# Kernel tuning notes

Hardware: AMD Instinct MI355X
Metric: run time of the kernel (lower is better)

## Reference

```python
import jax, jax.numpy as jnp
import numpy as np

N = 50000        # n_nodes
E = 640000       # n_edges
D = 128          # d_model (in_dim == out_dim)
H = 8            # num_heads
DH = D // H      # head dim = 16
EPS = 1e-5


def _batchnorm(x, g, b):
    # BatchNorm1d, training-mode batch statistics (biased variance)
    mu = jnp.mean(x, axis=0)
    var = jnp.mean((x - mu) ** 2, axis=0)
    return (x - mu) * jax.lax.rsqrt(var + EPS) * g + b


def setup_inputs() -> dict:
    key = jax.random.key(0)
    ks = jax.random.split(key, 16)
    s = 0.05
    h = jax.random.normal(ks[0], (N, D), jnp.float32)
    src = jax.random.randint(ks[1], (E,), 0, N)
    # guarantee every node has >= 1 incoming edge (avoids z == 0)
    dst = jnp.concatenate([jnp.arange(N), jax.random.randint(ks[2], (E - N,), 0, N)])
    return {
        "h": h,
        "src": src,
        "dst": dst,
        "WQ": jax.random.normal(ks[3], (D, D), jnp.float32) * s,
        "WK": jax.random.normal(ks[4], (D, D), jnp.float32) * s,
        "WV": jax.random.normal(ks[5], (D, D), jnp.float32) * s,
        "WO": jax.random.normal(ks[6], (D, D), jnp.float32) * s,
        "bO": jnp.zeros((D,), jnp.float32),
        "W1": jax.random.normal(ks[7], (2 * D, D), jnp.float32) * s,
        "b1": jnp.zeros((2 * D,), jnp.float32),
        "W2": jax.random.normal(ks[8], (D, 2 * D), jnp.float32) * s,
        "b2": jnp.zeros((D,), jnp.float32),
        "bn1_g": jnp.ones((D,), jnp.float32),
        "bn1_b": jnp.zeros((D,), jnp.float32),
        "bn2_g": jnp.ones((D,), jnp.float32),
        "bn2_b": jnp.zeros((D,), jnp.float32),
    }


def reference(h, src, dst, WQ, WK, WV, WO, bO, W1, b1, W2, b2, bn1_g, bn1_b, bn2_g, bn2_b):
    n = h.shape[0]
    # projections -> [N, H, DH]
    Q = (h @ WQ.T).reshape(n, H, DH)
    K = (h @ WK.T).reshape(n, H, DH)
    V = (h @ WV.T).reshape(n, H, DH)
    # per-edge score: sum(K[src] * Q[dst]) -> [E, H]; clamp/exp (scaled_exp)
    score = jnp.sum(K[src] * Q[dst], axis=-1) / np.sqrt(DH)
    score = jnp.exp(jnp.clip(score, -5.0, 5.0))
    # scatter-sum weighted values and normalizers to destination nodes
    wV = jax.ops.segment_sum(V[src] * score[..., None], dst, num_segments=n)  # [N,H,DH]
    z = jax.ops.segment_sum(score, dst, num_segments=n)                       # [N,H]
    attn = (wV / z[..., None]).reshape(n, D)
    # O projection + residual + BN1
    h1 = _batchnorm(h + (attn @ WO.T + bO), bn1_g, bn1_b)
    # FFN + residual + BN2
    f = jax.nn.relu(h1 @ W1.T + b1) @ W2.T + b2
    return _batchnorm(h1 + f, bn2_g, bn2_b)
```

## Files before the change

### kernel.cpp

```cpp
#include <hip/hip_runtime.h>
#include <math.h>


#define ND128 16384
typedef _Float16 f16;
typedef __attribute__((ext_vector_type(8))) _Float16 h8;
typedef __attribute__((ext_vector_type(4))) _Float16 h4;
typedef __attribute__((ext_vector_type(2))) _Float16 h2;
typedef __attribute__((ext_vector_type(4))) float f4;
typedef __attribute__((ext_vector_type(2))) float ff2;

__device__ __forceinline__ float fast_exp2(float x) {
#if __has_builtin(__builtin_amdgcn_exp2f)
    return __builtin_amdgcn_exp2f(x);
#else
    return exp2f(x);
#endif
}

template <int CTRL>
__device__ __forceinline__ float dppadd(float x) {
    int t = __builtin_amdgcn_update_dpp(0, __float_as_int(x), CTRL, 0xF, 0xF, false);
    return x + __int_as_float(t);
}
__device__ __forceinline__ float wsum8(float p) {
    p = dppadd<0xB1>(p);
    p = dppadd<0x4E>(p);
    p = dppadd<0x141>(p);
    return p;
}

__device__ __forceinline__ ff2 fp8x2_dec(unsigned v) {
#if __has_builtin(__builtin_amdgcn_cvt_pk_f32_fp8)
    return __builtin_amdgcn_cvt_pk_f32_fp8((int)v, false);
#else
    ff2 r;
    unsigned b0 = v & 0xffu, b1 = (v >> 8) & 0xffu;
    {
        unsigned e = (b0 >> 3) & 15u, m = b0 & 7u;
        float x = e ? __uint_as_float(((e + 120u) << 23) | (m << 20)) : (float)m * 0.001953125f;
        r.x = (b0 & 0x80u) ? -x : x;
    }
    {
        unsigned e = (b1 >> 3) & 15u, m = b1 & 7u;
        float x = e ? __uint_as_float(((e + 120u) << 23) | (m << 20)) : (float)m * 0.001953125f;
        r.y = (b1 & 0x80u) ? -x : x;
    }
    return r;
#endif
}

#if !__has_builtin(__builtin_amdgcn_cvt_pk_fp8_f32)
__device__ __forceinline__ unsigned char fp8_1(float f) {
    float a = fabsf(f);
    unsigned sg = (__float_as_uint(f) >> 31) << 7;
    if (a >= 448.f) return (unsigned char)(sg | 0x7E);
    if (a < 0.0009765625f) return (unsigned char)sg;
    int E; float m = frexpf(a, &E);
    if (E - 1 < -6) {
        int q = (int)rintf(a * 512.f);
        if (q > 7) return (unsigned char)(sg | 0x08);
        return (unsigned char)(sg | q);
    }
    int q = (int)rintf(m * 16.f);
    if (q == 16) { q = 8; E += 1; }
    int Ef = E - 1 + 7;
    if (Ef > 15) return (unsigned char)(sg | 0x7E);
    return (unsigned char)(sg | (Ef << 3) | (q - 8));
}
#endif

__device__ __forceinline__ unsigned fp8_pack4(float a0, float a1, float a2, float a3) {
#if __has_builtin(__builtin_amdgcn_cvt_pk_fp8_f32)
    int pk = __builtin_amdgcn_cvt_pk_fp8_f32(a0, a1, 0, false);
    pk = __builtin_amdgcn_cvt_pk_fp8_f32(a2, a3, pk, true);
    return (unsigned)pk;
#else
    return (unsigned)fp8_1(a0) | ((unsigned)fp8_1(a1) << 8) |
           ((unsigned)fp8_1(a2) << 16) | ((unsigned)fp8_1(a3) << 24);
#endif
}

__global__ __launch_bounds__(256) void k_prep_hist(
    const float* __restrict__ h, f16* __restrict__ hb,
    const float* __restrict__ WQ, const float* __restrict__ WK,
    const float* __restrict__ WV, const float* __restrict__ WO,
    const float* __restrict__ W2,
    f16* __restrict__ Wqb, f16* __restrict__ Wkb,
    f16* __restrict__ Wvb, f16* __restrict__ Wob, f16* __restrict__ W2b,
    int* __restrict__ cursor, const int* __restrict__ dst,
    int N, int E, int nhb)
{
    const int tid = threadIdx.x;
    if (blockIdx.x < (unsigned)nhb) {
        int e = blockIdx.x * 256 + tid;
        if (e < E) atomicAdd(&cursor[dst[e]], 1);
        return;
    }
    const int p = blockIdx.x - nhb;
    const int slab = p >> 1, my = p & 1;
#pragma unroll
    for (int it2 = 0; it2 < 4; ++it2) {
        int it = my * 4 + it2;
        int cid = it * 256 + tid;
        int lane = cid & 63;
        int m = (cid >> 6) & 7;
        int kb = cid >> 9;
        int row = slab * 128 + m * 16 + (lane & 15);
        int col = kb * 32 + (lane >> 4) * 8;
        f16 o8[8];
        if (row < N) {
            const float* pp = h + (size_t)row * 128 + col;
            float4 f0 = *(const float4*)pp;
            float4 f1 = *(const float4*)(pp + 4);
            o8[0] = (f16)f0.x; o8[1] = (f16)f0.y; o8[2] = (f16)f0.z; o8[3] = (f16)f0.w;
            o8[4] = (f16)f1.x; o8[5] = (f16)f1.y; o8[6] = (f16)f1.z; o8[7] = (f16)f1.w;
        } else {
#pragma unroll
            for (int j = 0; j < 8; ++j) o8[j] = (f16)0.f;
        }
        *(h8*)(hb + (size_t)slab * ND128 + (size_t)cid * 8) = *(const h8*)o8;
    }
    if (slab < 6 && my == 1) {
        const float* Wsrc; f16* dstw; int K, base;
        if (slab < 4) {
            Wsrc = slab == 0 ? WQ : slab == 1 ? WK : slab == 2 ? WV : WO;
            dstw = slab == 0 ? Wqb : slab == 1 ? Wkb : slab == 2 ? Wvb : Wob;
            K = 128; base = 0;
        } else {
            Wsrc = W2; dstw = W2b; K = 256; base = (slab - 4) * 2048;
        }
#pragma unroll
        for (int it = 0; it < 8; ++it) {
            int cid = base + it * 256 + tid;
            int lane = cid & 63;
            int kb, nt;
            if (K == 128) { kb = (cid >> 6) & 3; nt = cid >> 8; }
            else          { kb = (cid >> 6) & 7; nt = cid >> 9; }
            int row = nt * 16 + (lane & 15);
            int col = kb * 32 + (lane >> 4) * 8;
            const float* pp = Wsrc + (size_t)row * K + col;
            f16 o8[8];
#pragma unroll
            for (int j = 0; j < 8; ++j) o8[j] = (f16)pp[j];
            *(h8*)(dstw + (size_t)cid * 8) = *(const h8*)o8;
        }
    }
}

__global__ __launch_bounds__(256) void k_qkv(
    const f16* __restrict__ hb, const f16* __restrict__ Wqb,
    const f16* __restrict__ Wkb, const f16* __restrict__ Wvb,
    f16* __restrict__ Qb, unsigned char* __restrict__ KV8, int N)
{
    const int slab = blockIdx.x, oidx = blockIdx.y;
    const int w = threadIdx.x >> 6, lane = threadIdx.x & 63;
    const f16* __restrict__ Wb = oidx == 0 ? Wqb : oidx == 1 ? Wkb : Wvb;
    const f16* A = hb + (size_t)slab * ND128;

    h8 bfr[2][4];
#pragma unroll
    for (int nt = 0; nt < 2; ++nt)
#pragma unroll
        for (int kb = 0; kb < 4; ++kb)
            bfr[nt][kb] = *(const h8*)(Wb + (size_t)(((2 * w + nt) * 4 + kb) * 64 + lane) * 8);

    f4 acc[8][2];
    f4 zero = {0.f, 0.f, 0.f, 0.f};
#pragma unroll
    for (int m = 0; m < 8; ++m) { acc[m][0] = zero; acc[m][1] = zero; }

#pragma unroll
    for (int m = 0; m < 8; ++m) {
#pragma unroll
        for (int kb = 0; kb < 4; ++kb) {
            h8 a = *(const h8*)(A + (size_t)((kb * 8 + m) * 64 + lane) * 8);
            acc[m][0] = __builtin_amdgcn_mfma_f32_16x16x32_f16(bfr[0][kb], a, acc[m][0], 0, 0, 0);
            acc[m][1] = __builtin_amdgcn_mfma_f32_16x16x32_f16(bfr[1][kb], a, acc[m][1], 0, 0, 0);
        }
    }

    const int rl = lane & 15, quad = lane >> 4;
    if (oidx == 0) {
#pragma unroll
        for (int m = 0; m < 8; ++m) {
            int gr = slab * 128 + m * 16 + rl;
            if (gr < N) {
#pragma unroll
                for (int nt = 0; nt < 2; ++nt) {
                    h4 o;
                    o[0] = (f16)acc[m][nt][0]; o[1] = (f16)acc[m][nt][1];
                    o[2] = (f16)acc[m][nt][2]; o[3] = (f16)acc[m][nt][3];
                    *(h4*)(Qb + (size_t)gr * 128 + w * 32 + nt * 16 + quad * 4) = o;
                }
            }
        }
    } else {
        const int voff = (oidx == 2) ? 128 : 0;
#pragma unroll
        for (int m = 0; m < 8; ++m) {
            int gr = slab * 128 + m * 16 + rl;
            if (gr < N) {
#pragma unroll
                for (int nt = 0; nt < 2; ++nt) {
                    unsigned pk = fp8_pack4(acc[m][nt][0], acc[m][nt][1],
                                            acc[m][nt][2], acc[m][nt][3]);
                    *(unsigned*)(KV8 + (size_t)gr * 256 + voff + w * 32 + nt * 16 + quad * 4) = pk;
                }
            }
        }
    }
}

__global__ __launch_bounds__(256) void k_scanA(
    const int* __restrict__ cnt, int* __restrict__ bsum, int N)
{
    const int t = threadIdx.x;
    int base = blockIdx.x * 2048 + t * 8;
    int s = 0;
#pragma unroll
    for (int j = 0; j < 8; ++j) {
        int idx = base + j;
        if (idx < N) s += cnt[idx];
    }
#pragma unroll
    for (int off = 32; off; off >>= 1) s += __shfl_down(s, off, 64);
    __shared__ int ws4[4];
    if ((t & 63) == 0) ws4[t >> 6] = s;
    __syncthreads();
    if (t == 0) bsum[blockIdx.x] = ws4[0] + ws4[1] + ws4[2] + ws4[3];
}

__global__ __launch_bounds__(256) void k_scanC(
    const int* __restrict__ cnt, const int* __restrict__ bsum,
    int* __restrict__ rowptr, int* __restrict__ cursor, int N, int nsb)
{
    const int t = threadIdx.x, b = blockIdx.x;
    __shared__ int sboff;
    if (t == 0) {
        int r = 0;
        for (int i2 = 0; i2 < b; ++i2) r += bsum[i2];
        sboff = r;
    }
    if (t == 64 && b == nsb - 1) {
        int r = 0;
        for (int i2 = 0; i2 < nsb; ++i2) r += bsum[i2];
        rowptr[N] = r;
    }
    int base = b * 2048 + t * 8;
    int loc[8];
    int s = 0;
#pragma unroll
    for (int j = 0; j < 8; ++j) {
        int idx = base + j;
        loc[j] = (idx < N) ? cnt[idx] : 0;
        s += loc[j];
    }
    __shared__ int part[256];
    part[t] = s;
    __syncthreads();
    for (int off = 1; off < 256; off <<= 1) {
        int v = (t >= off) ? part[t - off] : 0;
        __syncthreads();
        part[t] += v;
        __syncthreads();
    }
    int run = sboff + (t ? part[t - 1] : 0);
#pragma unroll
    for (int j = 0; j < 8; ++j) {
        int idx = base + j;
        if (idx < N) { rowptr[idx] = run; cursor[idx] = run; run += loc[j]; }
    }
}

__global__ __launch_bounds__(256) void k_scatter(
    const int* __restrict__ src, const int* __restrict__ dst,
    int* __restrict__ cursor, int* __restrict__ csr_src, int E)
{
    int e = blockIdx.x * 256 + threadIdx.x;
    if (e < E) {
        int pos = atomicAdd(&cursor[dst[e]], 1);
        csr_src[pos] = src[e];
    }
}

__global__ __launch_bounds__(256) void k_attn(
    const f16* __restrict__ Qb, const unsigned char* __restrict__ KV8,
    const int* __restrict__ rowptr, const int* __restrict__ csr_src,
    f16* __restrict__ attnf, int N)
{
    const int node = blockIdx.x * 4 + (threadIdx.x >> 6);
    const int lane = threadIdx.x & 63;
    if (node >= N) return;
    const int beg = rowptr[node], end = rowptr[node + 1];

    float qx, qy;
    {
        h2 q2 = ((const h2*)(Qb + (size_t)node * 128))[lane];
        const float SCL = 0.25f * 1.44269504f;
        qx = (float)q2[0] * SCL;
        qy = (float)q2[1] * SCL;
    }
    const float CLP = 5.f * 1.44269504f;

    float axA = 0.f, ayA = 0.f, axB = 0.f, ayB = 0.f, zA = 0.f, zB = 0.f;
    int i = beg;
    for (; i + 3 < end; i += 4) {
        int s0 = csr_src[i], s1 = csr_src[i + 1];
        int s2 = csr_src[i + 2], s3 = csr_src[i + 3];
        unsigned k0 = *(const unsigned short*)(KV8 + (size_t)s0 * 256 + 2 * lane);
        unsigned k1 = *(const unsigned short*)(KV8 + (size_t)s1 * 256 + 2 * lane);
        unsigned k2 = *(const unsigned short*)(KV8 + (size_t)s2 * 256 + 2 * lane);
        unsigned k3 = *(const unsigned short*)(KV8 + (size_t)s3 * 256 + 2 * lane);
        unsigned v0 = *(const unsigned short*)(KV8 + (size_t)s0 * 256 + 128 + 2 * lane);
        unsigned v1 = *(const unsigned short*)(KV8 + (size_t)s1 * 256 + 128 + 2 * lane);
        unsigned v2 = *(const unsigned short*)(KV8 + (size_t)s2 * 256 + 128 + 2 * lane);
        unsigned v3 = *(const unsigned short*)(KV8 + (size_t)s3 * 256 + 128 + 2 * lane);
        ff2 kf0 = fp8x2_dec(k0), kf1 = fp8x2_dec(k1);
        ff2 kf2 = fp8x2_dec(k2), kf3 = fp8x2_dec(k3);
        float p0 = fmaf(qx, kf0.x, qy * kf0.y);
        float p1 = fmaf(qx, kf1.x, qy * kf1.y);
        float p2 = fmaf(qx, kf2.x, qy * kf2.y);
        float p3 = fmaf(qx, kf3.x, qy * kf3.y);
        p0 = wsum8(p0); p1 = wsum8(p1); p2 = wsum8(p2); p3 = wsum8(p3);
        float sc0 = fast_exp2(fminf(fmaxf(p0, -CLP), CLP));
        float sc1 = fast_exp2(fminf(fmaxf(p1, -CLP), CLP));
        float sc2 = fast_exp2(fminf(fmaxf(p2, -CLP), CLP));
        float sc3 = fast_exp2(fminf(fmaxf(p3, -CLP), CLP));
        ff2 vf0 = fp8x2_dec(v0), vf1 = fp8x2_dec(v1);
        ff2 vf2 = fp8x2_dec(v2), vf3 = fp8x2_dec(v3);
        axA = fmaf(vf0.x, sc0, axA); ayA = fmaf(vf0.y, sc0, ayA);
        axB = fmaf(vf1.x, sc1, axB); ayB = fmaf(vf1.y, sc1, ayB);
        axA = fmaf(vf2.x, sc2, axA); ayA = fmaf(vf2.y, sc2, ayA);
        axB = fmaf(vf3.x, sc3, axB); ayB = fmaf(vf3.y, sc3, ayB);
        zA += sc0 + sc2; zB += sc1 + sc3;
    }
    for (; i < end; ++i) {
        int s0 = csr_src[i];
        unsigned k0 = *(const unsigned short*)(KV8 + (size_t)s0 * 256 + 2 * lane);
        unsigned v0 = *(const unsigned short*)(KV8 + (size_t)s0 * 256 + 128 + 2 * lane);
        ff2 kf0 = fp8x2_dec(k0);
        float p0 = fmaf(qx, kf0.x, qy * kf0.y);
        p0 = wsum8(p0);
        float sc0 = fast_exp2(fminf(fmaxf(p0, -CLP), CLP));
        ff2 vf0 = fp8x2_dec(v0);
        axA = fmaf(vf0.x, sc0, axA); ayA = fmaf(vf0.y, sc0, ayA);
        zA += sc0;
    }
    float inv = 1.f / (zA + zB);
    h2 o2;
    o2[0] = (f16)((axA + axB) * inv);
    o2[1] = (f16)((ayA + ayB) * inv);
    int slab = node >> 7, m = (node >> 4) & 7, lr = node & 15;
    int kb = lane >> 4, quad2 = (lane & 15) >> 2, j = (lane & 3) * 2;
    *(h2*)(attnf + (size_t)slab * ND128 +
           (size_t)(((kb * 8 + m) * 64 + lr + 16 * quad2) * 8 + j)) = o2;
}

__global__ __launch_bounds__(256) void k_oproj(
    const f16* __restrict__ attnf, const f16* __restrict__ Wob,
    const f16* __restrict__ hbf, const float* __restrict__ bO,
    f16* __restrict__ t1b, float* __restrict__ bn, int N)
{
    __shared__ float csum[128], csq[128];
    const int tid = threadIdx.x, slab = blockIdx.x;
    const int w = tid >> 6, lane = tid & 63;
    if (tid < 128) { csum[tid] = 0.f; csq[tid] = 0.f; }
    __syncthreads();
    const f16* A = attnf + (size_t)slab * ND128;
    const f16* HB = hbf + (size_t)slab * ND128;

    h8 bfr[2][4];
#pragma unroll
    for (int nt = 0; nt < 2; ++nt)
#pragma unroll
        for (int kb = 0; kb < 4; ++kb)
            bfr[nt][kb] = *(const h8*)(Wob + (size_t)(((2 * w + nt) * 4 + kb) * 64 + lane) * 8);

    f4 acc[8][2];
    f4 zero = {0.f, 0.f, 0.f, 0.f};
#pragma unroll
    for (int m = 0; m < 8; ++m) { acc[m][0] = zero; acc[m][1] = zero; }
#pragma unroll
    for (int m = 0; m < 8; ++m) {
#pragma unroll
        for (int kb = 0; kb < 4; ++kb) {
            h8 a = *(const h8*)(A + (size_t)((kb * 8 + m) * 64 + lane) * 8);
            acc[m][0] = __builtin_amdgcn_mfma_f32_16x16x32_f16(bfr[0][kb], a, acc[m][0], 0, 0, 0);
            acc[m][1] = __builtin_amdgcn_mfma_f32_16x16x32_f16(bfr[1][kb], a, acc[m][1], 0, 0, 0);
        }
    }

    const int rl = lane & 15, quad = lane >> 4;
    float4 bo[2];
#pragma unroll
    for (int nt = 0; nt < 2; ++nt)
        bo[nt] = *(const float4*)(bO + w * 32 + nt * 16 + quad * 4);
    float pcs[2][4], pcq[2][4];
#pragma unroll
    for (int nt = 0; nt < 2; ++nt)
#pragma unroll
        for (int r = 0; r < 4; ++r) { pcs[nt][r] = 0.f; pcq[nt][r] = 0.f; }

#pragma unroll
    for (int m = 0; m < 8; ++m) {
        int gr = slab * 128 + m * 16 + rl;
        if (gr < N) {
#pragma unroll
            for (int nt = 0; nt < 2; ++nt) {
                size_t fidx = (size_t)(((w * 8 + m) * 64 + (nt * 2 + (quad >> 1)) * 16 + rl) * 8 +
                                       (quad & 1) * 4);
                h4 hv4 = *(const h4*)(HB + fidx);
                float v0 = acc[m][nt][0] + (float)hv4[0] + bo[nt].x;
                float v1 = acc[m][nt][1] + (float)hv4[1] + bo[nt].y;
                float v2 = acc[m][nt][2] + (float)hv4[2] + bo[nt].z;
                float v3 = acc[m][nt][3] + (float)hv4[3] + bo[nt].w;
                h4 o; o[0] = (f16)v0; o[1] = (f16)v1; o[2] = (f16)v2; o[3] = (f16)v3;
                *(h4*)(t1b + (size_t)slab * ND128 + fidx) = o;
                pcs[nt][0] += v0; pcq[nt][0] += v0 * v0;
                pcs[nt][1] += v1; pcq[nt][1] += v1 * v1;
                pcs[nt][2] += v2; pcq[nt][2] += v2 * v2;
                pcs[nt][3] += v3; pcq[nt][3] += v3 * v3;
            }
        }
    }
#pragma unroll
    for (int nt = 0; nt < 2; ++nt)
#pragma unroll
        for (int r = 0; r < 4; ++r) {
            float s = pcs[nt][r], q = pcq[nt][r];
            s += __shfl_xor(s, 8, 16); q += __shfl_xor(q, 8, 16);
            s += __shfl_xor(s, 4, 16); q += __shfl_xor(q, 4, 16);
            s += __shfl_xor(s, 2, 16); q += __shfl_xor(q, 2, 16);
            s += __shfl_xor(s, 1, 16); q += __shfl_xor(q, 1, 16);
            if (rl == 0) {
                int cl = w * 32 + nt * 16 + quad * 4 + r;
                atomicAdd(&csum[cl], s);
                atomicAdd(&csq[cl], q);
            }
        }
    __syncthreads();
    if (tid < 128) {
        atomicAdd(bn + tid, csum[tid]);
        atomicAdd(bn + 128 + tid, csq[tid]);
    }
}

__global__ __launch_bounds__(128) void k_fold1(
    const float* __restrict__ bn, const float* __restrict__ g1,
    const float* __restrict__ bb1, const float* __restrict__ W1,
    const float* __restrict__ b1, f16* __restrict__ W1b,
    float* __restrict__ badj, float* __restrict__ sfold,
    float* __restrict__ bfold, int N)
{
    const int o = blockIdx.x, i = threadIdx.x;
    float invN = 1.f / (float)N;
    float mu = bn[i] * invN;
    float var = bn[128 + i] * invN - mu * mu;
    float s = g1[i] * rsqrtf(var + 1e-5f);
    float bb = bb1[i] - mu * s;
    if (o == 0) { sfold[i] = s; bfold[i] = bb; }
    float wv = W1[(size_t)o * 128 + i];
    __shared__ float red[128];
    red[i] = wv * bb;
    const int nt = o >> 4, lanelow = o & 15;
    const int kb = i >> 5, quad = (i >> 3) & 3, j = i & 7;
    W1b[(size_t)(((nt * 4 + kb) * 64 + lanelow + 16 * quad) * 8 + j)] = (f16)(wv * s);
    __syncthreads();
#pragma unroll
    for (int off = 64; off; off >>= 1) {
        if (i < off) red[i] += red[i + off];
        __syncthreads();
    }
    if (i == 0) badj[o] = b1[o] + red[0];
}

__global__ __launch_bounds__(256) void k_ffn1(
    const f16* __restrict__ t1b, const f16* __restrict__ W1b,
    const float* __restrict__ badj, f16* __restrict__ ub, int N)
{
    const int slab = blockIdx.x, ch = blockIdx.y;
    const int w = threadIdx.x >> 6, lane = threadIdx.x & 63;
    const f16* A = t1b + (size_t)slab * ND128;

    h8 bfr[2][4];
#pragma unroll
    for (int nt = 0; nt < 2; ++nt)
#pragma unroll
        for (int kb = 0; kb < 4; ++kb) {
            int ntg = ch * 8 + 2 * w + nt;
            bfr[nt][kb] = *(const h8*)(W1b + (size_t)((ntg * 4 + kb) * 64 + lane) * 8);
        }

    f4 acc[8][2];
    f4 zero = {0.f, 0.f, 0.f, 0.f};
#pragma unroll
    for (int m = 0; m < 8; ++m) { acc[m][0] = zero; acc[m][1] = zero; }
#pragma unroll
    for (int m = 0; m < 8; ++m) {
#pragma unroll
        for (int kb = 0; kb < 4; ++kb) {
            h8 a = *(const h8*)(A + (size_t)((kb * 8 + m) * 64 + lane) * 8);
            acc[m][0] = __builtin_amdgcn_mfma_f32_16x16x32_f16(bfr[0][kb], a, acc[m][0], 0, 0, 0);
            acc[m][1] = __builtin_amdgcn_mfma_f32_16x16x32_f16(bfr[1][kb], a, acc[m][1], 0, 0, 0);
        }
    }

    const int rl = lane & 15, quad = lane >> 4;
    const int kbu = ch * 4 + w;
    float4 ba[2];
#pragma unroll
    for (int nt = 0; nt < 2; ++nt)
        ba[nt] = *(const float4*)(badj + ch * 128 + w * 32 + nt * 16 + quad * 4);
#pragma unroll
    for (int m = 0; m < 8; ++m) {
        int gr = slab * 128 + m * 16 + rl;
        if (gr < N) {
#pragma unroll
            for (int nt = 0; nt < 2; ++nt) {
                h4 o;
                o[0] = (f16)fmaxf(acc[m][nt][0] + ba[nt].x, 0.f);
                o[1] = (f16)fmaxf(acc[m][nt][1] + ba[nt].y, 0.f);
                o[2] = (f16)fmaxf(acc[m][nt][2] + ba[nt].z, 0.f);
                o[3] = (f16)fmaxf(acc[m][nt][3] + ba[nt].w, 0.f);
                *(h4*)(ub + (size_t)slab * 32768 +
                       (size_t)(((kbu * 8 + m) * 64 + (nt * 2 + (quad >> 1)) * 16 + rl) * 8 +
                                (quad & 1) * 4)) = o;
            }
        }
    }
}

__global__ __launch_bounds__(256) void k_ffn2(
    const f16* __restrict__ ub, const f16* __restrict__ W2b,
    const f16* __restrict__ t1b,
    const float* __restrict__ sfold, const float* __restrict__ bfold,
    const float* __restrict__ b2, f16* __restrict__ t2f,
    float* __restrict__ bn, int N)
{
    __shared__ float csum[128], csq[128], sS[128], sB[128];
    const int tid = threadIdx.x, slab = blockIdx.x;
    const int w = tid >> 6, lane = tid & 63;
    if (tid < 128) {
        csum[tid] = 0.f; csq[tid] = 0.f;
        sS[tid] = sfold[tid]; sB[tid] = bfold[tid] + b2[tid];
    }
    __syncthreads();
    const f16* A = ub + (size_t)slab * 32768;
    const f16* T1 = t1b + (size_t)slab * ND128;

    h8 bfr[2][8];
#pragma unroll
    for (int nt = 0; nt < 2; ++nt)
#pragma unroll
        for (int kb = 0; kb < 8; ++kb)
            bfr[nt][kb] = *(const h8*)(W2b + (size_t)(((2 * w + nt) * 8 + kb) * 64 + lane) * 8);

    f4 acc[8][2];
    f4 zero = {0.f, 0.f, 0.f, 0.f};
#pragma unroll
    for (int m = 0; m < 8; ++m) { acc[m][0] = zero; acc[m][1] = zero; }
#pragma unroll
    for (int m = 0; m < 8; ++m) {
#pragma unroll
        for (int kb = 0; kb < 8; ++kb) {
            h8 a = *(const h8*)(A + (size_t)((kb * 8 + m) * 64 + lane) * 8);
            acc[m][0] = __builtin_amdgcn_mfma_f32_16x16x32_f16(bfr[0][kb], a, acc[m][0], 0, 0, 0);
            acc[m][1] = __builtin_amdgcn_mfma_f32_16x16x32_f16(bfr[1][kb], a, acc[m][1], 0, 0, 0);
        }
    }

    const int rl = lane & 15, quad = lane >> 4;
    float pcs[2][4], pcq[2][4];
#pragma unroll
    for (int nt = 0; nt < 2; ++nt)
#pragma unroll
        for (int r = 0; r < 4; ++r) { pcs[nt][r] = 0.f; pcq[nt][r] = 0.f; }

#pragma unroll
    for (int m = 0; m < 8; ++m) {
        int gr = slab * 128 + m * 16 + rl;
        if (gr < N) {
#pragma unroll
            for (int nt = 0; nt < 2; ++nt) {
                int col0 = w * 32 + nt * 16 + quad * 4;
                size_t fidx = (size_t)(((w * 8 + m) * 64 + (nt * 2 + (quad >> 1)) * 16 + rl) * 8 +
                                       (quad & 1) * 4);
                h4 t1v = *(const h4*)(T1 + fidx);
                float4 ss = *(const float4*)&sS[col0];
                float4 sb = *(const float4*)&sB[col0];
                h4 o2;
                o2[0] = (f16)(acc[m][nt][0] + fmaf(ss.x, (float)t1v[0], sb.x));
                o2[1] = (f16)(acc[m][nt][1] + fmaf(ss.y, (float)t1v[1], sb.y));
                o2[2] = (f16)(acc[m][nt][2] + fmaf(ss.z, (float)t1v[2], sb.z));
                o2[3] = (f16)(acc[m][nt][3] + fmaf(ss.w, (float)t1v[3], sb.w));
                *(h4*)(t2f + (size_t)slab * ND128 + fidx) = o2;
                float r0 = (float)o2[0], r1 = (float)o2[1];
                float r2 = (float)o2[2], r3 = (float)o2[3];
                pcs[nt][0] += r0; pcq[nt][0] += r0 * r0;
                pcs[nt][1] += r1; pcq[nt][1] += r1 * r1;
                pcs[nt][2] += r2; pcq[nt][2] += r2 * r2;
                pcs[nt][3] += r3; pcq[nt][3] += r3 * r3;
            }
        }
    }
#pragma unroll
    for (int nt = 0; nt < 2; ++nt)
#pragma unroll
        for (int r = 0; r < 4; ++r) {
            float s = pcs[nt][r], q = pcq[nt][r];
            s += __shfl_xor(s, 8, 16); q += __shfl_xor(q, 8, 16);
            s += __shfl_xor(s, 4, 16); q += __shfl_xor(q, 4, 16);
            s += __shfl_xor(s, 2, 16); q += __shfl_xor(q, 2, 16);
            s += __shfl_xor(s, 1, 16); q += __shfl_xor(q, 1, 16);
            if (rl == 0) {
                int cl = w * 32 + nt * 16 + quad * 4 + r;
                atomicAdd(&csum[cl], s);
                atomicAdd(&csq[cl], q);
            }
        }
    __syncthreads();
    if (tid < 128) {
        atomicAdd(bn + 256 + tid, csum[tid]);
        atomicAdd(bn + 384 + tid, csq[tid]);
    }
}

__global__ __launch_bounds__(256) void k_bn2(
    const f16* __restrict__ t2f, float* __restrict__ out,
    const float* __restrict__ bn,
    const float* __restrict__ g2, const float* __restrict__ bb2, int N)
{
    __shared__ float sS[128], sB[128];
    const int tid = threadIdx.x;
    if (tid < 128) {
        float invN = 1.f / (float)N;
        float mu = bn[256 + tid] * invN;
        float var = bn[384 + tid] * invN - mu * mu;
        float scl = g2[tid] * rsqrtf(var + 1e-5f);
        sS[tid] = scl;
        sB[tid] = bb2[tid] - mu * scl;
    }
    __syncthreads();
    size_t idx = (size_t)blockIdx.x * 256 + tid;
    size_t total = (size_t)N * 32;
    if (idx < total) {
        int gr = (int)(idx >> 5);
        int c0 = ((int)idx & 31) * 4;
        int slab = gr >> 7, m = (gr >> 4) & 7, rl = gr & 15;
        int w = c0 >> 5, nt = (c0 >> 4) & 1, q = (c0 >> 2) & 3;
        size_t fidx = (size_t)(((w * 8 + m) * 64 + (nt * 2 + (q >> 1)) * 16 + rl) * 8 +
                               (q & 1) * 4);
        h4 v = *(const h4*)(t2f + (size_t)slab * ND128 + fidx);
        float4 o;
        o.x = fmaf((float)v[0], sS[c0 + 0], sB[c0 + 0]);
        o.y = fmaf((float)v[1], sS[c0 + 1], sB[c0 + 1]);
        o.z = fmaf((float)v[2], sS[c0 + 2], sB[c0 + 2]);
        o.w = fmaf((float)v[3], sS[c0 + 3], sB[c0 + 3]);
        *(float4*)(out + (size_t)gr * 128 + c0) = o;
    }
}

extern "C" void kernel_launch(void* const* d_in, const int* in_sizes, int n_in,
                              void* d_out, int out_size, void* d_ws, size_t ws_size,
                              hipStream_t stream)
{
    const float* h   = (const float*)d_in[0];
    const int*   src = (const int*)d_in[1];
    const int*   dst = (const int*)d_in[2];
    const float* WQ  = (const float*)d_in[3];
    const float* WK  = (const float*)d_in[4];
    const float* WV  = (const float*)d_in[5];
    const float* WO  = (const float*)d_in[6];
    const float* bO  = (const float*)d_in[7];
    const float* W1  = (const float*)d_in[8];
    const float* b1  = (const float*)d_in[9];
    const float* W2  = (const float*)d_in[10];
    const float* b2  = (const float*)d_in[11];
    const float* g1  = (const float*)d_in[12];
    const float* bb1 = (const float*)d_in[13];
    const float* g2  = (const float*)d_in[14];
    const float* bb2 = (const float*)d_in[15];
    float* out = (float*)d_out;

    int N = in_sizes[0] / 128;
    int E = in_sizes[1];
    int slabs = (N + 127) / 128;
    int nsb = (N + 2047) / 2048;
    int nhb = (E + 255) / 256;
    const size_t B1 = (size_t)slabs * 32768;

    char* Wp = (char*)d_ws;
    f16* hb  = (f16*)Wp;
    f16* Qb  = (f16*)(Wp + B1);
    unsigned char* KV8 = (unsigned char*)(Wp + 2 * B1);
    f16* attnf = (f16*)(Wp + 3 * B1);
    f16* t1b = (f16*)(Wp + 4 * B1);
    f16* ub  = (f16*)(Wp + B1);
    f16* t2f = attnf;
    const size_t base = 5 * B1;
    f16* Wqb = (f16*)(Wp + base);
    f16* Wkb = (f16*)(Wp + base + 32768);
    f16* Wvb = (f16*)(Wp + base + 65536);
    f16* Wob = (f16*)(Wp + base + 98304);
    f16* W1b = (f16*)(Wp + base + 131072);
    f16* W2b = (f16*)(Wp + base + 196608);
    float* badj  = (float*)(Wp + base + 262144);
    float* sfold = (float*)(Wp + base + 263168);
    float* bfold = (float*)(Wp + base + 263680);
    float* bn    = (float*)(Wp + base + 264192);
    int* bsum    = (int*)(Wp + base + 266240);
    int* cursor  = (int*)(Wp + base + 266496);
    int* rowptr  = (int*)(Wp + base + 266496 + (size_t)N * 4);
    int* csr     = (int*)(Wp + base + 266496 + (size_t)N * 8 + 8);

    hipMemsetAsync(Wp + base + 264192, 0, 2304 + (size_t)N * 4, stream);
    k_prep_hist<<<nhb + slabs * 2, 256, 0, stream>>>(
        h, hb, WQ, WK, WV, WO, W2, Wqb, Wkb, Wvb, Wob, W2b, cursor, dst, N, E, nhb);
    k_qkv<<<dim3(slabs, 3), 256, 0, stream>>>(hb, Wqb, Wkb, Wvb, Qb, KV8, N);
    k_scanA<<<nsb, 256, 0, stream>>>(cursor, bsum, N);
    k_scanC<<<nsb, 256, 0, stream>>>(cursor, bsum, rowptr, cursor, N, nsb);
    k_scatter<<<nhb, 256, 0, stream>>>(src, dst, cursor, csr, E);
    k_attn<<<(N + 3) / 4, 256, 0, stream>>>(Qb, KV8, rowptr, csr, attnf, N);
    k_oproj<<<slabs, 256, 0, stream>>>(attnf, Wob, hb, bO, t1b, bn, N);
    k_fold1<<<256, 128, 0, stream>>>(bn, g1, bb1, W1, b1, W1b, badj, sfold, bfold, N);
    k_ffn1<<<dim3(slabs, 2), 256, 0, stream>>>(t1b, W1b, badj, ub, N);
    k_ffn2<<<slabs, 256, 0, stream>>>(ub, W2b, t1b, sfold, bfold, b2, t2f, bn, N);
    k_bn2<<<(int)(((size_t)N * 32 + 255) / 256), 256, 0, stream>>>(t2f, out, bn, g2, bb2, N);
}
```

Measured before the change: 308.4 us.

## Interleave fp8 K/V per lane and unroll edge gather loop by eight

The K and V fp8 rows are now stored interleaved, so each lane's two K bytes and two V bytes sit in one 4-byte word. The attention kernel then fetches K and V for an edge with a single 32-bit gather instead of two 16-bit gathers. The main edge loop is unrolled to eight edges, with a four-edge tail, so more loads are in flight per wave. The cost is more registers per thread and narrower 16-bit stores in the projection epilogue.

```diff
diff --git a/kernel.cpp b/kernel.cpp
--- a/kernel.cpp
+++ b/kernel.cpp
@@ -30,10 +30,7 @@
     return p;
 }
 
-__device__ __forceinline__ ff2 fp8x2_dec(unsigned v) {
-#if __has_builtin(__builtin_amdgcn_cvt_pk_f32_fp8)
-    return __builtin_amdgcn_cvt_pk_f32_fp8((int)v, false);
-#else
+__device__ __forceinline__ ff2 fp8x2_dec_sw(unsigned v) {
     ff2 r;
     unsigned b0 = v & 0xffu, b1 = (v >> 8) & 0xffu;
     {
@@ -47,6 +44,20 @@
         r.y = (b1 & 0x80u) ? -x : x;
     }
     return r;
+}
+
+__device__ __forceinline__ ff2 dec_lo(unsigned v) {
+#if __has_builtin(__builtin_amdgcn_cvt_pk_f32_fp8)
+    return __builtin_amdgcn_cvt_pk_f32_fp8((int)v, false);
+#else
+    return fp8x2_dec_sw(v & 0xffffu);
+#endif
+}
+__device__ __forceinline__ ff2 dec_hi(unsigned v) {
+#if __has_builtin(__builtin_amdgcn_cvt_pk_f32_fp8)
+    return __builtin_amdgcn_cvt_pk_f32_fp8((int)v, true);
+#else
+    return fp8x2_dec_sw((v >> 16) & 0xffffu);
 #endif
 }
 
@@ -70,14 +81,12 @@
 }
 #endif
 
-__device__ __forceinline__ unsigned fp8_pack4(float a0, float a1, float a2, float a3) {
+__device__ __forceinline__ unsigned short fp8_pack2(float a0, float a1) {
 #if __has_builtin(__builtin_amdgcn_cvt_pk_fp8_f32)
     int pk = __builtin_amdgcn_cvt_pk_fp8_f32(a0, a1, 0, false);
-    pk = __builtin_amdgcn_cvt_pk_fp8_f32(a2, a3, pk, true);
-    return (unsigned)pk;
+    return (unsigned short)(pk & 0xffff);
 #else
-    return (unsigned)fp8_1(a0) | ((unsigned)fp8_1(a1) << 8) |
-           ((unsigned)fp8_1(a2) << 16) | ((unsigned)fp8_1(a3) << 24);
+    return (unsigned short)((unsigned)fp8_1(a0) | ((unsigned)fp8_1(a1) << 8));
 #endif
 }
 
@@ -196,16 +205,19 @@
             }
         }
     } else {
-        const int voff = (oidx == 2) ? 128 : 0;
+        const int koff = (oidx == 2) ? 2 : 0;
 #pragma unroll
         for (int m = 0; m < 8; ++m) {
             int gr = slab * 128 + m * 16 + rl;
             if (gr < N) {
 #pragma unroll
                 for (int nt = 0; nt < 2; ++nt) {
-                    unsigned pk = fp8_pack4(acc[m][nt][0], acc[m][nt][1],
-                                            acc[m][nt][2], acc[m][nt][3]);
-                    *(unsigned*)(KV8 + (size_t)gr * 256 + voff + w * 32 + nt * 16 + quad * 4) = pk;
+                    int c0 = w * 32 + nt * 16 + quad * 4;
+                    unsigned short p01 = fp8_pack2(acc[m][nt][0], acc[m][nt][1]);
+                    unsigned short p23 = fp8_pack2(acc[m][nt][2], acc[m][nt][3]);
+                    unsigned char* rowp = KV8 + (size_t)gr * 256 + (size_t)c0 * 2 + koff;
+                    *(unsigned short*)(rowp) = p01;
+                    *(unsigned short*)(rowp + 4) = p23;
                 }
             }
         }
@@ -302,49 +314,70 @@
         qy = (float)q2[1] * SCL;
     }
     const float CLP = 5.f * 1.44269504f;
+    const unsigned loff = 4u * (unsigned)lane;
 
     float axA = 0.f, ayA = 0.f, axB = 0.f, ayB = 0.f, zA = 0.f, zB = 0.f;
     int i = beg;
-    for (; i + 3 < end; i += 4) {
-        int s0 = csr_src[i], s1 = csr_src[i + 1];
-        int s2 = csr_src[i + 2], s3 = csr_src[i + 3];
-        unsigned k0 = *(const unsigned short*)(KV8 + (size_t)s0 * 256 + 2 * lane);
-        unsigned k1 = *(const unsigned short*)(KV8 + (size_t)s1 * 256 + 2 * lane);
-        unsigned k2 = *(const unsigned short*)(KV8 + (size_t)s2 * 256 + 2 * lane);
-        unsigned k3 = *(const unsigned short*)(KV8 + (size_t)s3 * 256 + 2 * lane);
-        unsigned v0 = *(const unsigned short*)(KV8 + (size_t)s0 * 256 + 128 + 2 * lane);
-        unsigned v1 = *(const unsigned short*)(KV8 + (size_t)s1 * 256 + 128 + 2 * lane);
-        unsigned v2 = *(const unsigned short*)(KV8 + (size_t)s2 * 256 + 128 + 2 * lane);
-        unsigned v3 = *(const unsigned short*)(KV8 + (size_t)s3 * 256 + 128 + 2 * lane);
-        ff2 kf0 = fp8x2_dec(k0), kf1 = fp8x2_dec(k1);
-        ff2 kf2 = fp8x2_dec(k2), kf3 = fp8x2_dec(k3);
-        float p0 = fmaf(qx, kf0.x, qy * kf0.y);
-        float p1 = fmaf(qx, kf1.x, qy * kf1.y);
-        float p2 = fmaf(qx, kf2.x, qy * kf2.y);
-        float p3 = fmaf(qx, kf3.x, qy * kf3.y);
-        p0 = wsum8(p0); p1 = wsum8(p1); p2 = wsum8(p2); p3 = wsum8(p3);
-        float sc0 = fast_exp2(fminf(fmaxf(p0, -CLP), CLP));
-        float sc1 = fast_exp2(fminf(fmaxf(p1, -CLP), CLP));
-        float sc2 = fast_exp2(fminf(fmaxf(p2, -CLP), CLP));
-        float sc3 = fast_exp2(fminf(fmaxf(p3, -CLP), CLP));
-        ff2 vf0 = fp8x2_dec(v0), vf1 = fp8x2_dec(v1);
-        ff2 vf2 = fp8x2_dec(v2), vf3 = fp8x2_dec(v3);
-        axA = fmaf(vf0.x, sc0, axA); ayA = fmaf(vf0.y, sc0, ayA);
-        axB = fmaf(vf1.x, sc1, axB); ayB = fmaf(vf1.y, sc1, ayB);
-        axA = fmaf(vf2.x, sc2, axA); ayA = fmaf(vf2.y, sc2, ayA);
-        axB = fmaf(vf3.x, sc3, axB); ayB = fmaf(vf3.y, sc3, ayB);
-        zA += sc0 + sc2; zB += sc1 + sc3;
+    for (; i + 7 < end; i += 8) {
+        int s[8];
+#pragma unroll
+        for (int u = 0; u < 8; ++u) s[u] = csr_src[i + u];
+        unsigned kv[8];
+#pragma unroll
+        for (int u = 0; u < 8; ++u)
+            kv[u] = *(const unsigned*)(KV8 + (size_t)s[u] * 256 + loff);
+        float p[8];
+#pragma unroll
+        for (int u = 0; u < 8; ++u) {
+            ff2 kf = dec_lo(kv[u]);
+            p[u] = fmaf(qx, kf.x, qy * kf.y);
+        }
+#pragma unroll
+        for (int u = 0; u < 8; ++u) p[u] = wsum8(p[u]);
+        float sc[8];
+#pragma unroll
+        for (int u = 0; u < 8; ++u)
+            sc[u] = fast_exp2(fminf(fmaxf(p[u], -CLP), CLP));
+#pragma unroll
+        for (int u = 0; u < 8; ++u) {
+            ff2 vf = dec_hi(kv[u]);
+            if (u & 1) {
+                axB = fmaf(vf.x, sc[u], axB); ayB = fmaf(vf.y, sc[u], ayB); zB += sc[u];
+            } else {
+                axA = fmaf(vf.x, sc[u], axA); ayA = fmaf(vf.y, sc[u], ayA); zA += sc[u];
+            }
+        }
+    }
+    if (i + 3 < end) {
+        int s[4];
+#pragma unroll
+        for (int u = 0; u < 4; ++u) s[u] = csr_src[i + u];
+        unsigned kv[4];
+#pragma unroll
+        for (int u = 0; u < 4; ++u)
+            kv[u] = *(const unsigned*)(KV8 + (size_t)s[u] * 256 + loff);
+#pragma unroll
+        for (int u = 0; u < 4; ++u) {
+            ff2 kf = dec_lo(kv[u]);
+            float p = wsum8(fmaf(qx, kf.x, qy * kf.y));
+            float scu = fast_exp2(fminf(fmaxf(p, -CLP), CLP));
+            ff2 vf = dec_hi(kv[u]);
+            if (u & 1) {
+                axB = fmaf(vf.x, scu, axB); ayB = fmaf(vf.y, scu, ayB); zB += scu;
+            } else {
+                axA = fmaf(vf.x, scu, axA); ayA = fmaf(vf.y, scu, ayA); zA += scu;
+            }
+        }
+        i += 4;
     }
     for (; i < end; ++i) {
         int s0 = csr_src[i];
-        unsigned k0 = *(const unsigned short*)(KV8 + (size_t)s0 * 256 + 2 * lane);
-        unsigned v0 = *(const unsigned short*)(KV8 + (size_t)s0 * 256 + 128 + 2 * lane);
-        ff2 kf0 = fp8x2_dec(k0);
-        float p0 = fmaf(qx, kf0.x, qy * kf0.y);
-        p0 = wsum8(p0);
+        unsigned kv = *(const unsigned*)(KV8 + (size_t)s0 * 256 + loff);
+        ff2 kf = dec_lo(kv);
+        float p0 = wsum8(fmaf(qx, kf.x, qy * kf.y));
         float sc0 = fast_exp2(fminf(fmaxf(p0, -CLP), CLP));
-        ff2 vf0 = fp8x2_dec(v0);
-        axA = fmaf(vf0.x, sc0, axA); ayA = fmaf(vf0.y, sc0, ayA);
+        ff2 vf = dec_hi(kv);
+        axA = fmaf(vf.x, sc0, axA); ayA = fmaf(vf.y, sc0, ayA);
         zA += sc0;
     }
     float inv = 1.f / (zA + zB);
```

New measurement: 310.4 us. About the same (+0.6%).
